# Kernel tuning notes

Hardware: AMD Instinct MI355X
Metric: run time of the kernel (lower is better)

Reference implementation:

```python
import jax, jax.numpy as jnp
import numpy as np

# 47 skeleton edges (parent, child) from getSkeletalModelStructure()
EDGES = np.array([
    (0, 1), (1, 2), (2, 3), (3, 29), (1, 5), (5, 6), (6, 8), (8, 9), (8, 13),
    (8, 17), (8, 21), (8, 25), (9, 10), (10, 11), (11, 12), (13, 14), (14, 15),
    (15, 16), (17, 18), (18, 19), (19, 20), (21, 22), (22, 23), (23, 24),
    (25, 26), (26, 27), (27, 28), (29, 30), (29, 34), (29, 38), (29, 42),
    (29, 46), (30, 31), (31, 32), (32, 33), (34, 35), (35, 36), (36, 37),
    (38, 39), (39, 40), (40, 41), (42, 43), (43, 44), (44, 45), (46, 47),
    (47, 48), (48, 49)], dtype=np.int32)

N_JOINTS = 50
N_EDGES = 47


def _length_direct(pose):
    # pose: [B, T, 151]; drop counter channel, view as joints
    B, T = pose.shape[0], pose.shape[1]
    p = pose[..., :-1].reshape(B, T, N_JOINTS, 3)
    diff = p[:, :, EDGES[:, 0], :] - p[:, :, EDGES[:, 1], :]   # [B, T, 47, 3]
    length = jnp.linalg.norm(diff, axis=-1)                      # [B, T, 47]
    eps = jnp.finfo(pose.dtype).tiny
    direct = diff / (length + eps)[..., None]                    # [B, T, 47, 3]
    # torch stacks each [B,T,3] edge dir along dim=-1 -> [B,T,3,47], then reshapes
    directs = jnp.transpose(direct, (0, 1, 3, 2)).reshape(B, T, N_EDGES * 3)
    return length, directs


def setup_inputs() -> dict:
    key = jax.random.key(0)
    k1, k2 = jax.random.split(key)
    B, T, D = 128, 1024, 151
    preds = jax.random.normal(k1, (B, T, D), dtype=jnp.float32)
    targets = jax.random.normal(k2, (B, T, D), dtype=jnp.float32)
    return {"preds": preds, "targets": targets}


def reference(preds, targets):
    target_pad = 0.0
    mask = (targets != target_pad).astype(preds.dtype)           # [B, T, 151]
    preds_m = preds * mask
    targets_m = targets * mask
    _, preds_dir = _length_direct(preds_m)
    _, targets_dir = _length_direct(targets_m)
    preds_dir = preds_dir * mask[:, :, :N_EDGES * 3]
    targets_dir = targets_dir * mask[:, :, :N_EDGES * 3]
    # cfg: loss='l1' (mean abs), vel_loss='mse' (mean square), loss_scale=1.0
    l1 = jnp.mean(jnp.abs(preds_m - targets_m))
    vel_mse = jnp.mean(jnp.square(preds_dir - targets_dir))
    return l1 + 0.1 * vel_mse
```

## Files before the change

kernel.cpp:

```cpp
#include <hip/hip_runtime.h>


#define N_ROWS   (128 * 1024)
#define ROW      151
#define N_EDGES  47
#define GRID     2048
#define BLOCK    256
#define CHUNKS   4
#define CHUNK_ROWS 4
#define CHUNK_DW (CHUNK_ROWS * ROW)
#define CHUNK_TASKS (CHUNK_ROWS * N_EDGES)
#define BUF_DW (2 * CHUNK_DW)

#if __has_builtin(__builtin_amdgcn_rsqf)
__device__ __forceinline__ float fast_rsq(float x) { return __builtin_amdgcn_rsqf(x); }
#else
__device__ __forceinline__ float fast_rsq(float x) {
    float r; asm volatile("v_rsq_f32 %0, %1" : "=v"(r) : "v"(x)); return r;
}
#endif

__device__ __forceinline__ float4 ldg4(const float* __restrict__ p) {
    return *reinterpret_cast<const float4*>(p);
}
__device__ __forceinline__ void st4(float* __restrict__ p, float4 v) {
    *reinterpret_cast<float4*>(p) = v;
}

#define E(p, c) ((unsigned)((p) * 3) | ((unsigned)((c) * 3) << 16))
__constant__ unsigned c_edge[N_EDGES] = {
    E(0,1),  E(1,2),  E(2,3),  E(3,29), E(1,5),  E(5,6),  E(6,8),  E(8,9),
    E(8,13), E(8,17), E(8,21), E(8,25), E(9,10), E(10,11),E(11,12),E(13,14),
    E(14,15),E(15,16),E(17,18),E(18,19),E(19,20),E(21,22),E(22,23),E(23,24),
    E(25,26),E(26,27),E(27,28),E(29,30),E(29,34),E(29,38),E(29,42),E(29,46),
    E(30,31),E(31,32),E(32,33),E(34,35),E(35,36),E(36,37),E(38,39),E(39,40),
    E(40,41),E(42,43),E(43,44),E(44,45),E(46,47),E(47,48),E(48,49)};

struct EdgeAddr { int aP[3], aC[3], aM[3]; };

__device__ __forceinline__ void acc_l1(float4 pv, float4 tv, float& l1) {
    float a0 = (tv.x != 0.f) ? pv.x : 0.f;
    float a1 = (tv.y != 0.f) ? pv.y : 0.f;
    float a2 = (tv.z != 0.f) ? pv.z : 0.f;
    float a3 = (tv.w != 0.f) ? pv.w : 0.f;
    l1 += fabsf(a0 - tv.x) + fabsf(a1 - tv.y)
        + fabsf(a2 - tv.z) + fabsf(a3 - tv.w);
}

__device__ __forceinline__ void compute_edges(
        const float* __restrict__ B, const EdgeAddr& ea, int lane, float& vel) {
    const float* __restrict__ Bp = B;
    const float* __restrict__ Bt = B + CHUNK_DW;
#pragma unroll
    for (int k = 0; k < 3; ++k) {
        if (k < 2 || lane < (CHUNK_TASKS - 128)) {
            int aP = ea.aP[k], aC = ea.aC[k], aM = ea.aM[k];
            float tpx = Bt[aP], tpy = Bt[aP + 1], tpz = Bt[aP + 2];
            float tcx = Bt[aC], tcy = Bt[aC + 1], tcz = Bt[aC + 2];
            float ppx = Bp[aP], ppy = Bp[aP + 1], ppz = Bp[aP + 2];
            float pcx = Bp[aC], pcy = Bp[aC + 1], pcz = Bp[aC + 2];
            float apx = (tpx != 0.f) ? ppx : 0.f;
            float apy = (tpy != 0.f) ? ppy : 0.f;
            float apz = (tpz != 0.f) ? ppz : 0.f;
            float acx = (tcx != 0.f) ? pcx : 0.f;
            float acy = (tcy != 0.f) ? pcy : 0.f;
            float acz = (tcz != 0.f) ? pcz : 0.f;
            float pdx = apx - acx, pdy = apy - acy, pdz = apz - acz;
            float tdx = tpx - tcx, tdy = tpy - tcy, tdz = tpz - tcz;
            float pd2 = pdx * pdx + pdy * pdy + pdz * pdz;
            float td2 = tdx * tdx + tdy * tdy + tdz * tdz;
            float pinv = (pd2 > 0.f) ? fast_rsq(pd2) : 0.f;
            float tinv = (td2 > 0.f) ? fast_rsq(td2) : 0.f;
            float dx = pdx * pinv - tdx * tinv;
            float dy = pdy * pinv - tdy * tinv;
            float dz = pdz * pinv - tdz * tinv;
            float m0 = (Bt[aM]      != 0.f) ? 1.f : 0.f;
            float m1 = (Bt[aM + 47] != 0.f) ? 1.f : 0.f;
            float m2 = (Bt[aM + 94] != 0.f) ? 1.f : 0.f;
            vel += m0 * dx * dx + m1 * dy * dy + m2 * dz * dz;
        }
    }
}

__global__ __launch_bounds__(BLOCK, 4) void reg_loss_main(
        const float* __restrict__ preds, const float* __restrict__ targets,
        float* __restrict__ wsL, float* __restrict__ wsV) {
    __shared__ float S[4][BUF_DW];
    __shared__ float redL[4], redV[4];

    const int t = threadIdx.x;
    const int lane = t & 63;
    const int wave = t >> 6;
    float* B = &S[wave][0];

    const long long wb =
        (long long)(blockIdx.x * 4 + wave) * (CHUNKS * CHUNK_DW);
    const float* gp = preds + wb;
    const float* gt = targets + wb;

    const int l4 = lane * 4;
    const bool tail = lane < 23;
    const int off2 = tail ? (512 + l4) : l4;

    EdgeAddr ea;
#pragma unroll
    for (int k = 0; k < 3; ++k) {
        int task = lane + k * 64;
        bool a = task < CHUNK_TASKS;
        int r = a ? task / N_EDGES : 0;
        int e = a ? task - r * N_EDGES : 0;
        int roff = r * ROW;
        unsigned pk = c_edge[e];
        ea.aP[k] = roff + (int)(pk & 0xffff);
        ea.aC[k] = roff + (int)(pk >> 16);
        ea.aM[k] = roff + e;
    }

    float l1 = 0.f, vel = 0.f;
    float4 p0, p1, p2, t0, t1, t2;

    p0 = ldg4(gp + l4);       p1 = ldg4(gp + 256 + l4);
    t0 = ldg4(gt + l4);       t1 = ldg4(gt + 256 + l4);
    p2 = ldg4(gp + off2);     t2 = ldg4(gt + off2);

#pragma unroll
    for (int c = 0; c < CHUNKS; ++c) {
        st4(B + l4,                  p0);
        st4(B + 256 + l4,            p1);
        st4(B + CHUNK_DW + l4,       t0);
        st4(B + CHUNK_DW + 256 + l4, t1);
        if (tail) {
            st4(B + 512 + l4,            p2);
            st4(B + CHUNK_DW + 512 + l4, t2);
        }

        acc_l1(p0, t0, l1);
        acc_l1(p1, t1, l1);
        if (tail) acc_l1(p2, t2, l1);

        if (c + 1 < CHUNKS) {
            const float* cp = gp + (c + 1) * CHUNK_DW;
            const float* ct = gt + (c + 1) * CHUNK_DW;
            p0 = ldg4(cp + l4);       p1 = ldg4(cp + 256 + l4);
            t0 = ldg4(ct + l4);       t1 = ldg4(ct + 256 + l4);
            p2 = ldg4(cp + off2);     t2 = ldg4(ct + off2);
        }
        __builtin_amdgcn_sched_barrier(0);

        compute_edges(B, ea, lane, vel);
    }

#pragma unroll
    for (int off = 32; off > 0; off >>= 1) {
        l1  += __shfl_down(l1, off);
        vel += __shfl_down(vel, off);
    }
    if (lane == 0) { redL[wave] = l1; redV[wave] = vel; }
    __syncthreads();
    if (t == 0) {
        wsL[blockIdx.x] = redL[0] + redL[1] + redL[2] + redL[3];
        wsV[blockIdx.x] = redV[0] + redV[1] + redV[2] + redV[3];
    }
}

__global__ __launch_bounds__(BLOCK) void reg_loss_finalize(
        const float* __restrict__ wsL, const float* __restrict__ wsV,
        float* __restrict__ out) {
    __shared__ double rl[4], rv[4];
    const int t = threadIdx.x;
    const int lane = t & 63;
    const int wave = t >> 6;
    double L = 0.0, V = 0.0;
    for (int k = t; k < GRID; k += BLOCK) { L += wsL[k]; V += wsV[k]; }
#pragma unroll
    for (int off = 32; off > 0; off >>= 1) {
        L += __shfl_down(L, off);
        V += __shfl_down(V, off);
    }
    if (lane == 0) { rl[wave] = L; rv[wave] = V; }
    __syncthreads();
    if (t == 0) {
        double Ls = rl[0] + rl[1] + rl[2] + rl[3];
        double Vs = rv[0] + rv[1] + rv[2] + rv[3];
        out[0] = (float)(Ls / ((double)N_ROWS * 151.0)
                       + 0.1 * (Vs / ((double)N_ROWS * 141.0)));
    }
}

extern "C" void kernel_launch(void* const* d_in, const int* in_sizes, int n_in,
                              void* d_out, int out_size, void* d_ws, size_t ws_size,
                              hipStream_t stream) {
    const float* preds   = (const float*)d_in[0];
    const float* targets = (const float*)d_in[1];
    float* wsL = (float*)d_ws;
    float* wsV = wsL + GRID;
    float* out = (float*)d_out;

    reg_loss_main<<<GRID, BLOCK, 0, stream>>>(preds, targets, wsL, wsV);
    reg_loss_finalize<<<1, BLOCK, 0, stream>>>(wsL, wsV, out);
}
```

Before: 178.6 us.

## Drop LDS staging and gather edge joints directly from global memory

```diff
diff --git a/kernel.cpp b/kernel.cpp
--- a/kernel.cpp
+++ b/kernel.cpp
@@ -6,11 +6,12 @@
 #define N_EDGES  47
 #define GRID     2048
 #define BLOCK    256
-#define CHUNKS   4
-#define CHUNK_ROWS 4
-#define CHUNK_DW (CHUNK_ROWS * ROW)
-#define CHUNK_TASKS (CHUNK_ROWS * N_EDGES)
-#define BUF_DW (2 * CHUNK_DW)
+#define ROWS_PER_BLOCK 64
+#define SUBS     4
+#define SUB_ROWS 16
+#define SUB_DW   (SUB_ROWS * ROW)
+#define SUB_F4   (SUB_DW / 4)
+#define SUB_TASKS (SUB_ROWS * N_EDGES)
 
 #if __has_builtin(__builtin_amdgcn_rsqf)
 __device__ __forceinline__ float fast_rsq(float x) { return __builtin_amdgcn_rsqf(x); }
@@ -20,11 +21,9 @@
 }
 #endif
 
-__device__ __forceinline__ float4 ldg4(const float* __restrict__ p) {
-    return *reinterpret_cast<const float4*>(p);
-}
-__device__ __forceinline__ void st4(float* __restrict__ p, float4 v) {
-    *reinterpret_cast<float4*>(p) = v;
+struct f3 { float x, y, z; };
+__device__ __forceinline__ f3 ldg3(const float* __restrict__ p) {
+    return *reinterpret_cast<const f3*>(p);
 }
 
 #define E(p, c) ((unsigned)((p) * 3) | ((unsigned)((c) * 3) << 16))
@@ -47,66 +46,53 @@
         + fabsf(a2 - tv.z) + fabsf(a3 - tv.w);
 }
 
-__device__ __forceinline__ void compute_edges(
-        const float* __restrict__ B, const EdgeAddr& ea, int lane, float& vel) {
-    const float* __restrict__ Bp = B;
-    const float* __restrict__ Bt = B + CHUNK_DW;
-#pragma unroll
-    for (int k = 0; k < 3; ++k) {
-        if (k < 2 || lane < (CHUNK_TASKS - 128)) {
-            int aP = ea.aP[k], aC = ea.aC[k], aM = ea.aM[k];
-            float tpx = Bt[aP], tpy = Bt[aP + 1], tpz = Bt[aP + 2];
-            float tcx = Bt[aC], tcy = Bt[aC + 1], tcz = Bt[aC + 2];
-            float ppx = Bp[aP], ppy = Bp[aP + 1], ppz = Bp[aP + 2];
-            float pcx = Bp[aC], pcy = Bp[aC + 1], pcz = Bp[aC + 2];
-            float apx = (tpx != 0.f) ? ppx : 0.f;
-            float apy = (tpy != 0.f) ? ppy : 0.f;
-            float apz = (tpz != 0.f) ? ppz : 0.f;
-            float acx = (tcx != 0.f) ? pcx : 0.f;
-            float acy = (tcy != 0.f) ? pcy : 0.f;
-            float acz = (tcz != 0.f) ? pcz : 0.f;
-            float pdx = apx - acx, pdy = apy - acy, pdz = apz - acz;
-            float tdx = tpx - tcx, tdy = tpy - tcy, tdz = tpz - tcz;
-            float pd2 = pdx * pdx + pdy * pdy + pdz * pdz;
-            float td2 = tdx * tdx + tdy * tdy + tdz * tdz;
-            float pinv = (pd2 > 0.f) ? fast_rsq(pd2) : 0.f;
-            float tinv = (td2 > 0.f) ? fast_rsq(td2) : 0.f;
-            float dx = pdx * pinv - tdx * tinv;
-            float dy = pdy * pinv - tdy * tinv;
-            float dz = pdz * pinv - tdz * tinv;
-            float m0 = (Bt[aM]      != 0.f) ? 1.f : 0.f;
-            float m1 = (Bt[aM + 47] != 0.f) ? 1.f : 0.f;
-            float m2 = (Bt[aM + 94] != 0.f) ? 1.f : 0.f;
-            vel += m0 * dx * dx + m1 * dy * dy + m2 * dz * dz;
-        }
-    }
+__device__ __forceinline__ void edge_task(
+        const float* __restrict__ bp, const float* __restrict__ bt,
+        int aP, int aC, int aM, float& vel) {
+    f3 tp = ldg3(bt + aP);
+    f3 tc = ldg3(bt + aC);
+    f3 pp = ldg3(bp + aP);
+    f3 pc = ldg3(bp + aC);
+    float mg0 = bt[aM], mg1 = bt[aM + 47], mg2 = bt[aM + 94];
+    float apx = (tp.x != 0.f) ? pp.x : 0.f;
+    float apy = (tp.y != 0.f) ? pp.y : 0.f;
+    float apz = (tp.z != 0.f) ? pp.z : 0.f;
+    float acx = (tc.x != 0.f) ? pc.x : 0.f;
+    float acy = (tc.y != 0.f) ? pc.y : 0.f;
+    float acz = (tc.z != 0.f) ? pc.z : 0.f;
+    float pdx = apx - acx, pdy = apy - acy, pdz = apz - acz;
+    float tdx = tp.x - tc.x, tdy = tp.y - tc.y, tdz = tp.z - tc.z;
+    float pd2 = pdx * pdx + pdy * pdy + pdz * pdz;
+    float td2 = tdx * tdx + tdy * tdy + tdz * tdz;
+    float pinv = (pd2 > 0.f) ? fast_rsq(pd2) : 0.f;
+    float tinv = (td2 > 0.f) ? fast_rsq(td2) : 0.f;
+    float dx = pdx * pinv - tdx * tinv;
+    float dy = pdy * pinv - tdy * tinv;
+    float dz = pdz * pinv - tdz * tinv;
+    float m0 = (mg0 != 0.f) ? 1.f : 0.f;
+    float m1 = (mg1 != 0.f) ? 1.f : 0.f;
+    float m2 = (mg2 != 0.f) ? 1.f : 0.f;
+    vel += m0 * dx * dx + m1 * dy * dy + m2 * dz * dz;
 }
 
 __global__ __launch_bounds__(BLOCK, 4) void reg_loss_main(
         const float* __restrict__ preds, const float* __restrict__ targets,
         float* __restrict__ wsL, float* __restrict__ wsV) {
-    __shared__ float S[4][BUF_DW];
     __shared__ float redL[4], redV[4];
 
     const int t = threadIdx.x;
     const int lane = t & 63;
     const int wave = t >> 6;
-    float* B = &S[wave][0];
 
-    const long long wb =
-        (long long)(blockIdx.x * 4 + wave) * (CHUNKS * CHUNK_DW);
-    const float* gp = preds + wb;
-    const float* gt = targets + wb;
-
-    const int l4 = lane * 4;
-    const bool tail = lane < 23;
-    const int off2 = tail ? (512 + l4) : l4;
+    const long long slab = (long long)blockIdx.x * (ROWS_PER_BLOCK * ROW);
+    const float* sp = preds + slab;
+    const float* st = targets + slab;
 
     EdgeAddr ea;
 #pragma unroll
     for (int k = 0; k < 3; ++k) {
-        int task = lane + k * 64;
-        bool a = task < CHUNK_TASKS;
+        int task = t + k * 256;
+        bool a = task < SUB_TASKS;
         int r = a ? task / N_EDGES : 0;
         int e = a ? task - r * N_EDGES : 0;
         int roff = r * ROW;
@@ -117,37 +103,30 @@
     }
 
     float l1 = 0.f, vel = 0.f;
-    float4 p0, p1, p2, t0, t1, t2;
-
-    p0 = ldg4(gp + l4);       p1 = ldg4(gp + 256 + l4);
-    t0 = ldg4(gt + l4);       t1 = ldg4(gt + 256 + l4);
-    p2 = ldg4(gp + off2);     t2 = ldg4(gt + off2);
 
 #pragma unroll
-    for (int c = 0; c < CHUNKS; ++c) {
-        st4(B + l4,                  p0);
-        st4(B + 256 + l4,            p1);
-        st4(B + CHUNK_DW + l4,       t0);
-        st4(B + CHUNK_DW + 256 + l4, t1);
-        if (tail) {
-            st4(B + 512 + l4,            p2);
-            st4(B + CHUNK_DW + 512 + l4, t2);
+    for (int sub = 0; sub < SUBS; ++sub) {
+        const float* __restrict__ bp = sp + sub * SUB_DW;
+        const float* __restrict__ bt = st + sub * SUB_DW;
+        const float4* __restrict__ bp4 = reinterpret_cast<const float4*>(bp);
+        const float4* __restrict__ bt4 = reinterpret_cast<const float4*>(bt);
+
+#pragma unroll
+        for (int k = 0; k < 3; ++k) {
+            int i = t + k * 256;
+            if (k < 2 || t < (SUB_F4 - 512)) {
+                float4 pv = bp4[i];
+                float4 tv = bt4[i];
+                acc_l1(pv, tv, l1);
+            }
         }
 
-        acc_l1(p0, t0, l1);
-        acc_l1(p1, t1, l1);
-        if (tail) acc_l1(p2, t2, l1);
-
-        if (c + 1 < CHUNKS) {
-            const float* cp = gp + (c + 1) * CHUNK_DW;
-            const float* ct = gt + (c + 1) * CHUNK_DW;
-            p0 = ldg4(cp + l4);       p1 = ldg4(cp + 256 + l4);
-            t0 = ldg4(ct + l4);       t1 = ldg4(ct + 256 + l4);
-            p2 = ldg4(cp + off2);     t2 = ldg4(ct + off2);
+#pragma unroll
+        for (int k = 0; k < 3; ++k) {
+            if (k < 2 || t < (SUB_TASKS - 512)) {
+                edge_task(bp, bt, ea.aP[k], ea.aC[k], ea.aM[k], vel);
+            }
         }
-        __builtin_amdgcn_sched_barrier(0);
-
-        compute_edges(B, ea, lane, vel);
     }
 
 #pragma unroll
```

Result: slower. 183.6 us (+2.8%).
